# Optimization experiments

Hardware: AMD Instinct MI355X
Metric: run time of the kernel (lower is better)

Reference implementation:

```python
import math
import jax, jax.numpy as jnp
import numpy as np

ORIG, NEW, LPW = 16000, 22050, 6  # orig_freq, new_freq, lowpass_filter_width


def _filters():
    """Kaldi LinearResample filter bank: first input index + weights per output phase.

    Mirrors Resample._indices_and_weights exactly (computed statically in numpy
    since the frequencies are module constants).
    """
    base = math.gcd(ORIG, NEW)
    P = NEW // base           # output_samples (number of polyphase filters)
    stride = ORIG // base     # conv_stride (input samples per polyphase block)
    cutoff = 0.99 * 0.5 * min(ORIG, NEW)
    ww = LPW / (2.0 * cutoff)  # half window width in seconds
    out_t = np.arange(P, dtype=np.float64) / NEW
    min_i = np.ceil((out_t - ww) * ORIG)   # first_indices, per phase
    max_i = np.floor((out_t + ww) * ORIG)
    W = int((max_i - min_i + 1).max())     # max filter length (~13 taps)
    j = np.arange(W, dtype=np.float64)
    inp_i = min_i[:, None] + j[None, :]
    dt = inp_i / ORIG - out_t[:, None]
    w = np.zeros_like(dt)
    inside = np.abs(dt) < ww
    w[inside] = 0.5 * (1.0 + np.cos(2.0 * np.pi * cutoff / LPW * dt[inside]))
    zero = dt == 0.0
    nz = ~zero
    w[nz] *= np.sin(2.0 * np.pi * cutoff * dt[nz]) / (np.pi * dt[nz])
    w[zero] *= 2.0 * cutoff
    w /= ORIG
    return min_i.astype(np.int64), w.astype(np.float32), P, stride


def _num_out(n):
    """Resample._output_samples (Kaldi GetNumOutputSamples)."""
    tick = ORIG * NEW // math.gcd(ORIG, NEW)
    tpi, tpo = tick // ORIG, tick // NEW
    interval = n * tpi
    if interval <= 0:
        return 0
    last = interval // tpo
    if last * tpo == interval:
        last -= 1
    return last + 1


def setup_inputs() -> dict:
    key = jax.random.key(0)
    # [batch, time] = 8 examples of 60 s @ 16 kHz
    return {"waveforms": jax.random.normal(key, (8, 960000), dtype=jnp.float32)}


def reference(waveforms):
    # Fused gather/dot formulation of the polyphase conv1d/conv_transpose1d loop:
    # out[b, t] = sum_j weights[t % P, j] * x[first_idx[t % P] + (t // P) * stride + j]
    # with zero padding outside [0, n) — bit-identical math to the torch loop.
    fi, w, P, stride = _filters()
    B, n = waveforms.shape
    tot = _num_out(n)
    Wn = w.shape[1]
    t = np.arange(tot)
    phase = t % P
    base = fi[phase] + (t // P) * stride           # [tot]
    full = base[:, None] + np.arange(Wn)[None, :]  # [tot, Wn] input sample indices
    pad_l = max(0, -int(full.min()))
    pad_r = max(0, int(full.max()) - (n - 1))
    xp = jnp.pad(waveforms, ((0, 0), (pad_l, pad_r)))
    idx = jnp.asarray(full + pad_l)                # static gather indices
    gathered = xp[:, idx]                          # [B, tot, Wn]
    wt = jnp.asarray(w)[phase]                     # [tot, Wn]
    return jnp.einsum('btw,tw->bt', gathered, wt)
```

## Files before the change

### kernel.cpp

```cpp
#include <hip/hip_runtime.h>
#include <math.h>

#define ORIG_F 16000
#define NEW_F  22050
#define LPW    6
#define P      441
#define STRIDE 320
#define W      13
#define GPW    3
#define NG     147
#define W20    20
#define MPT    12
#define MCH    250
#define BATCH  8

#ifndef M_PI
#define M_PI 3.14159265358979323846
#endif

__device__ __forceinline__ double kaldi_fi(int p, double* out_t) {
    const double cutoff = 0.99 * 0.5 * (double)ORIG_F;
    const double ww = (double)LPW / (2.0 * cutoff);
    double ot = (double)p / (double)NEW_F;
    *out_t = ot;
    return ceil((ot - ww) * (double)ORIG_F);
}

__global__ void build_table20_kernel(float* __restrict__ w20, int* __restrict__ gab) {
    int idx = blockIdx.x * blockDim.x + threadIdx.x;
    if (idx >= P * W20) return;
    int p = idx / W20;
    int j = idx - p * W20;
    const double cutoff = 0.99 * 0.5 * (double)ORIG_F;
    const double ww = (double)LPW / (2.0 * cutoff);
    double out_t, out_t0;
    double min_i = kaldi_fi(p, &out_t);
    int fi = (int)min_i;
    int p0 = (p / GPW) * GPW;
    int fi0 = (int)kaldi_fi(p0, &out_t0);
    int ab = fi0 & ~3;
    if (j == 0 && p == p0) gab[p / GPW] = ab;
    int jt = ab + j - fi;
    float wf = 0.f;
    if (jt >= 0 && jt < W) {
        double dt = (min_i + (double)jt) / (double)ORIG_F - out_t;
        double wv = 0.0;
        if (fabs(dt) < ww) {
            wv = 0.5 * (1.0 + cos(2.0 * M_PI * cutoff / (double)LPW * dt));
            if (dt != 0.0) wv *= sin(2.0 * M_PI * cutoff * dt) / (M_PI * dt);
            else           wv *= 2.0 * cutoff;
        }
        wv /= (double)ORIG_F;
        wf = (float)wv;
    }
    w20[p * W20 + j] = wf;
}

__device__ __forceinline__ float dot20(const float4& x0, const float4& x1,
                                       const float4& x2, const float4& x3,
                                       const float4& x4, const float4* w) {
    return x0.x*w[0].x + x0.y*w[0].y + x0.z*w[0].z + x0.w*w[0].w
         + x1.x*w[1].x + x1.y*w[1].y + x1.z*w[1].z + x1.w*w[1].w
         + x2.x*w[2].x + x2.y*w[2].y + x2.z*w[2].z + x2.w*w[2].w
         + x3.x*w[3].x + x3.y*w[3].y + x3.z*w[3].z + x3.w*w[3].w
         + x4.x*w[4].x + x4.y*w[4].y + x4.z*w[4].z + x4.w*w[4].w;
}

__global__ __launch_bounds__(256) void resample3_kernel(
    const float* __restrict__ x, const float* __restrict__ w20,
    const int* __restrict__ gab, float* __restrict__ out,
    int n, int tot)
{
    int tid = blockIdx.x * blockDim.x + threadIdx.x;
    int g    = tid % NG;
    int rest = tid / NG;
    int mc   = rest % MCH;
    int b    = rest / MCH;
    if (b >= BATCH) return;

    const float* __restrict__ xb = x + (size_t)b * n;
    float* __restrict__ ob = out + (size_t)b * tot;

    const float4* wp = (const float4*)(w20 + g * (GPW * W20));
    float4 w[15];
    #pragma unroll
    for (int i = 0; i < 15; ++i) w[i] = wp[i];
    const int ab = gab[g];
    const int m0 = mc * MPT;
    const int p0 = g * GPW;

    #pragma unroll 2
    for (int k = 0; k < MPT; ++k) {
        const int m = m0 + k;
        const int base = ab + m * STRIDE;
        float4 x0, x1, x2, x3, x4;
        if (base >= 0 && base + W20 <= n) {
            const float4* xp = (const float4*)(xb + base);
            x0 = xp[0]; x1 = xp[1]; x2 = xp[2]; x3 = xp[3]; x4 = xp[4];
        } else {
            float xs[W20];
            #pragma unroll
            for (int j = 0; j < W20; ++j) {
                int ii = base + j;
                xs[j] = (ii >= 0 && ii < n) ? xb[ii] : 0.f;
            }
            x0 = make_float4(xs[0], xs[1], xs[2], xs[3]);
            x1 = make_float4(xs[4], xs[5], xs[6], xs[7]);
            x2 = make_float4(xs[8], xs[9], xs[10], xs[11]);
            x3 = make_float4(xs[12], xs[13], xs[14], xs[15]);
            x4 = make_float4(xs[16], xs[17], xs[18], xs[19]);
        }
        float a0 = dot20(x0, x1, x2, x3, x4, &w[0]);
        float a1 = dot20(x0, x1, x2, x3, x4, &w[5]);
        float a2 = dot20(x0, x1, x2, x3, x4, &w[10]);
        const int t = m * P + p0;
        __builtin_nontemporal_store(a0, &ob[t]);
        __builtin_nontemporal_store(a1, &ob[t + 1]);
        __builtin_nontemporal_store(a2, &ob[t + 2]);
    }
}

extern "C" void kernel_launch(void* const* d_in, const int* in_sizes, int n_in,
                              void* d_out, int out_size, void* d_ws, size_t ws_size,
                              hipStream_t stream) {
    const float* x = (const float*)d_in[0];
    float* out = (float*)d_out;

    const int n = in_sizes[0] / BATCH;

    long long interval = (long long)n * P;
    long long last = interval / STRIDE;
    if (last * STRIDE == interval) last -= 1;
    const int tot = (int)(last + 1);

    float* w20 = (float*)d_ws;
    int*   gab = (int*)((char*)d_ws + (size_t)P * W20 * sizeof(float));

    build_table20_kernel<<<(P * W20 + 255) / 256, 256, 0, stream>>>(w20, gab);

    const long long nthreads = (long long)BATCH * MCH * NG;
    const int nblk = (int)((nthreads + 255) / 256);
    resample3_kernel<<<nblk, 256, 0, stream>>>(x, w20, gab, out, n, tot);
}
```

Measured before the change: 30.35 us.

## Stage input tile and output block in LDS with coalesced vector stores

Each 512-thread block now loads one contiguous input tile per batch row into shared memory with float4 loads. 441 threads compute the polyphase dot products from LDS and write the results into a shared output buffer. The whole block then streams that buffer to global memory with coalesced nontemporal float4 stores. This replaces the scattered per-thread global reads and the strided 3-float stores, which were poorly coalesced. In exchange the kernel uses more LDS, adds two barriers, and leaves 71 threads idle during compute.

```diff
diff --git a/kernel.cpp b/kernel.cpp
--- a/kernel.cpp
+++ b/kernel.cpp
@@ -10,13 +10,17 @@
 #define GPW    3
 #define NG     147
 #define W20    20
-#define MPT    12
-#define MCH    250
+#define MBLK   24
+#define MCH    125
 #define BATCH  8
+#define TILE_F 7700
+#define OUTT_F (MBLK * P)
 
 #ifndef M_PI
 #define M_PI 3.14159265358979323846
 #endif
+
+typedef float f4n __attribute__((ext_vector_type(4)));
 
 __device__ __forceinline__ double kaldi_fi(int p, double* out_t) {
     const double cutoff = 0.99 * 0.5 * (double)ORIG_F;
@@ -66,57 +70,72 @@
          + x4.x*w[4].x + x4.y*w[4].y + x4.z*w[4].z + x4.w*w[4].w;
 }
 
-__global__ __launch_bounds__(256) void resample3_kernel(
+__global__ __launch_bounds__(512, 4) void resample6_kernel(
     const float* __restrict__ x, const float* __restrict__ w20,
     const int* __restrict__ gab, float* __restrict__ out,
     int n, int tot)
 {
-    int tid = blockIdx.x * blockDim.x + threadIdx.x;
-    int g    = tid % NG;
-    int rest = tid / NG;
-    int mc   = rest % MCH;
-    int b    = rest / MCH;
-    if (b >= BATCH) return;
+    __shared__ float xt[TILE_F];
+    __shared__ float ot[OUTT_F];
 
+    const int b  = blockIdx.y;
+    const int mc = blockIdx.x;
     const float* __restrict__ xb = x + (size_t)b * n;
-    float* __restrict__ ob = out + (size_t)b * tot;
 
-    const float4* wp = (const float4*)(w20 + g * (GPW * W20));
+    const int S4 = mc * (MBLK * STRIDE) - 8;
+
+    for (int i4 = threadIdx.x; i4 < TILE_F / 4; i4 += 512) {
+        const int gi = S4 + i4 * 4;
+        float4 v;
+        if (gi >= 0 && gi + 3 < n) {
+            v = *(const float4*)(xb + gi);
+        } else {
+            float s[4];
+            #pragma unroll
+            for (int q = 0; q < 4; ++q) {
+                int ii = gi + q;
+                s[q] = (ii >= 0 && ii < n) ? xb[ii] : 0.f;
+            }
+            v = make_float4(s[0], s[1], s[2], s[3]);
+        }
+        *(float4*)(xt + i4 * 4) = v;
+    }
+
+    const int t = threadIdx.x;
     float4 w[15];
-    #pragma unroll
-    for (int i = 0; i < 15; ++i) w[i] = wp[i];
-    const int ab = gab[g];
-    const int m0 = mc * MPT;
-    const int p0 = g * GPW;
+    int Lbase = 0, obase = 0;
+    const bool active = (t < P);
+    if (active) {
+        const int g     = t % NG;
+        const int third = t / NG;
+        const float4* wp = (const float4*)(w20 + g * (GPW * W20));
+        #pragma unroll
+        for (int i = 0; i < 15; ++i) w[i] = wp[i];
+        Lbase = gab[g] + 8 + third * (8 * STRIDE);
+        obase = third * 8 * P + GPW * g;
+    }
+    __syncthreads();
 
-    #pragma unroll 2
-    for (int k = 0; k < MPT; ++k) {
-        const int m = m0 + k;
-        const int base = ab + m * STRIDE;
-        float4 x0, x1, x2, x3, x4;
-        if (base >= 0 && base + W20 <= n) {
-            const float4* xp = (const float4*)(xb + base);
-            x0 = xp[0]; x1 = xp[1]; x2 = xp[2]; x3 = xp[3]; x4 = xp[4];
-        } else {
-            float xs[W20];
-            #pragma unroll
-            for (int j = 0; j < W20; ++j) {
-                int ii = base + j;
-                xs[j] = (ii >= 0 && ii < n) ? xb[ii] : 0.f;
-            }
-            x0 = make_float4(xs[0], xs[1], xs[2], xs[3]);
-            x1 = make_float4(xs[4], xs[5], xs[6], xs[7]);
-            x2 = make_float4(xs[8], xs[9], xs[10], xs[11]);
-            x3 = make_float4(xs[12], xs[13], xs[14], xs[15]);
-            x4 = make_float4(xs[16], xs[17], xs[18], xs[19]);
+    if (active) {
+        #pragma unroll 1
+        for (int k = 0; k < 8; ++k) {
+            const float4* q4 = (const float4*)(xt + Lbase);
+            float4 x0 = q4[0], x1 = q4[1], x2 = q4[2], x3 = q4[3], x4 = q4[4];
+            float a0 = dot20(x0, x1, x2, x3, x4, &w[0]);
+            float a1 = dot20(x0, x1, x2, x3, x4, &w[5]);
+            float a2 = dot20(x0, x1, x2, x3, x4, &w[10]);
+            ot[obase]     = a0;
+            ot[obase + 1] = a1;
+            ot[obase + 2] = a2;
+            Lbase += STRIDE; obase += P;
         }
-        float a0 = dot20(x0, x1, x2, x3, x4, &w[0]);
-        float a1 = dot20(x0, x1, x2, x3, x4, &w[5]);
-        float a2 = dot20(x0, x1, x2, x3, x4, &w[10]);
-        const int t = m * P + p0;
-        __builtin_nontemporal_store(a0, &ob[t]);
-        __builtin_nontemporal_store(a1, &ob[t + 1]);
-        __builtin_nontemporal_store(a2, &ob[t + 2]);
+    }
+    __syncthreads();
+
+    float* __restrict__ dst = out + (size_t)b * tot + (size_t)mc * OUTT_F;
+    for (int i4 = threadIdx.x; i4 < OUTT_F / 4; i4 += 512) {
+        f4n v = *(const f4n*)(ot + i4 * 4);
+        __builtin_nontemporal_store(v, (f4n*)(dst + i4 * 4));
     }
 }
 
@@ -138,7 +157,6 @@
 
     build_table20_kernel<<<(P * W20 + 255) / 256, 256, 0, stream>>>(w20, gab);
 
-    const long long nthreads = (long long)BATCH * MCH * NG;
-    const int nblk = (int)((nthreads + 255) / 256);
-    resample3_kernel<<<nblk, 256, 0, stream>>>(x, w20, gab, out, n, tot);
+    dim3 grid(MCH, BATCH);
+    resample6_kernel<<<grid, 512, 0, stream>>>(x, w20, gab, out, n, tot);
 }
```

New measurement: 95.13 us. +213.4%, slower.
